# Optimization experiments

Measured on AMD Instinct MI355X. Metric: run time of the kernel, lower is better.

## Reference

```python
import jax, jax.numpy as jnp
import numpy as np

MEM_SIZE = 1_000_000
DIM = 128
BS = 256
K = 1024
TEMP = 0.07
MOM_V = 0.5
MOM_A = 0.5


def _l2norm(x, axis=-1, eps=1e-12):
    n = jnp.sqrt(jnp.sum(x * x, axis=axis, keepdims=True))
    return x / jnp.maximum(n, eps)


def setup_inputs() -> dict:
    key = jax.random.key(0)
    k1, k2, k3, k4, k5, k6 = jax.random.split(key, 6)
    video_emb = jax.random.normal(k1, (BS, DIM), dtype=jnp.float32)
    audio_emb = jax.random.normal(k2, (BS, DIM), dtype=jnp.float32)
    y = jax.random.randint(k3, (BS,), 0, MEM_SIZE, dtype=jnp.int32)
    # alias method draws over memory_size-1 items (before shifting past y)
    neg_idx = jax.random.randint(k4, (BS, K), 0, MEM_SIZE - 1, dtype=jnp.int32)
    view1_mem = _l2norm(jax.random.normal(k5, (MEM_SIZE, DIM), dtype=jnp.float32))
    view2_mem = _l2norm(jax.random.normal(k6, (MEM_SIZE, DIM), dtype=jnp.float32))
    return {
        "video_emb": video_emb,
        "audio_emb": audio_emb,
        "y": y,
        "neg_idx": neg_idx,
        "view1_mem": view1_mem,
        "view2_mem": view2_mem,
    }


def reference(video_emb, audio_emb, y, neg_idx, view1_mem, view2_mem):
    v = _l2norm(video_emb, axis=1)   # [bs, dim]
    a = _l2norm(audio_emb, axis=1)   # [bs, dim]

    # shift negative indices past the positive index y (as in sample_negatives)
    idx = neg_idx + (neg_idx >= y[:, None]).astype(neg_idx.dtype)  # [bs, K]

    # gather positives / negatives from memory banks
    v_pos = view1_mem[y]           # [bs, dim]
    a_pos = view2_mem[y]           # [bs, dim]
    v_neg = view1_mem[idx]         # [bs, K, dim]
    a_neg = view2_mem[idx]         # [bs, K, dim]

    # xModal scores (wModal=False)
    v2a_pos = jnp.einsum("bd,bd->b", a_pos, v)[:, None] / TEMP    # [bs, 1]
    v2a_neg = jnp.einsum("bkd,bd->bk", a_neg, v) / TEMP           # [bs, K]
    a2v_pos = jnp.einsum("bd,bd->b", v_pos, a)[:, None] / TEMP    # [bs, 1]
    a2v_neg = jnp.einsum("bkd,bd->bk", v_neg, a) / TEMP           # [bs, K]

    scores = jnp.stack(
        [jnp.concatenate([v2a_pos, v2a_neg], axis=1),
         jnp.concatenate([a2v_pos, a2v_neg], axis=1)],
        axis=0,
    )  # [2, bs, K+1]

    # momentum scatter update of memory banks (no_grad in original)
    new1 = _l2norm(MOM_V * v_pos + (1.0 - MOM_V) * v, axis=1)
    new2 = _l2norm(MOM_A * a_pos + (1.0 - MOM_A) * a, axis=1)
    view1_new = view1_mem.at[y].set(new1)
    view2_new = view2_mem.at[y].set(new2)

    return scores, view1_new, view2_new
```

## Files before the change

### kernel.cpp

```cpp
#include <hip/hip_runtime.h>

#define MEM_SIZE 1000000
#define DIM 128
#define BS 256
#define K 1024
#define NSC (K + 1)
#define CAP 4
#define OVFCAP 32768

constexpr float INV_TEMP = 1.0f / 0.07f;
constexpr float MOM = 0.5f;

#define NB 2048
#define BT 256
#define NWAVES (NB * BT / 64)

typedef float fx4 __attribute__((ext_vector_type(4)));

#define QTAB_OFF 0
#define CNT_OFF  262144
#define SLOT_OFF 4262144
#define OVFC_OFF 20262144
#define OVF_OFF  20262400
#define WS_NEED  20524544

__device__ __forceinline__ float wave_reduce_sum(float v) {
    #pragma unroll
    for (int off = 32; off > 0; off >>= 1)
        v += __shfl_xor(v, off, 64);
    return v;
}

__global__ void normzero_kernel(const float* __restrict__ video,
                                const float* __restrict__ audio,
                                float* __restrict__ qtab,
                                int* __restrict__ counts,
                                int* __restrict__ ovf_cnt) {
    const int u = blockIdx.x;
    const int lane = threadIdx.x;
    const int b = u & (BS - 1);
    const float* src = (u < BS) ? video : audio;
    const float2 e = reinterpret_cast<const float2*>(src + b * DIM)[lane];
    const float ss = wave_reduce_sum(e.x * e.x + e.y * e.y);
    const float inv = 1.0f / fmaxf(sqrtf(ss), 1e-12f);
    reinterpret_cast<float2*>(qtab + u * DIM)[lane] =
        make_float2(e.x * inv, e.y * inv);
    for (int i = u * 64 + lane; i < MEM_SIZE; i += 512 * 64) counts[i] = 0;
    if (u == 0 && lane == 0) *ovf_cnt = 0;
}

__global__ void build_kernel(const int* __restrict__ y,
                             const int* __restrict__ neg,
                             int* __restrict__ counts,
                             int* __restrict__ slots,
                             int* __restrict__ ovf_cnt,
                             int2* __restrict__ ovf) {
    const int E = blockIdx.x * blockDim.x + threadIdx.x;
    int b, j, row;
    if (E < BS * K) {
        b = E >> 10;
        const int jj = E & 1023;
        j = jj + 1;
        const int ni = neg[b * K + jj];
        const int yb = y[b];
        row = ni + (ni >= yb ? 1 : 0);
    } else {
        b = E - BS * K;
        if (b >= BS) return;
        j = 0;
        row = y[b];
    }
    const int key = (b << 11) | j;
    const int old = atomicAdd(&counts[row], 1);
    if (old < CAP) {
        slots[row * CAP + old] = key;
    } else {
        const int p = atomicAdd(ovf_cnt, 1);
        if (p < OVFCAP) ovf[p] = make_int2(row, key);
    }
}

__global__ __launch_bounds__(BT) void main_kernel(
    const float* __restrict__ view1, const float* __restrict__ view2,
    const float* __restrict__ qtab, const int* __restrict__ counts,
    const int* __restrict__ slots,
    float* __restrict__ scores,
    fx4* __restrict__ out1, fx4* __restrict__ out2) {
    const int tid = blockIdx.x * BT + threadIdx.x;
    const int wid = tid >> 6;
    const int lane = tid & 63;
    const int half = lane >> 5;
    const int hl = lane & 31;
    const fx4* s1 = reinterpret_cast<const fx4*>(view1);
    const fx4* s2 = reinterpret_cast<const fx4*>(view2);
    const fx4* qt4 = reinterpret_cast<const fx4*>(qtab);

    const long long n4 = (long long)MEM_SIZE * DIM / 4;
    for (long long wbase = (long long)wid * 64; wbase < n4;
         wbase += (long long)NWAVES * 64) {
        const long long i = wbase + lane;
        const fx4 a = s1[i];
        const fx4 c = s2[i];
        __builtin_nontemporal_store(a, &out1[i]);
        __builtin_nontemporal_store(c, &out2[i]);

        const int row = (int)(wbase >> 5) + half;
        int cnt = counts[row];
        if (cnt > CAP) cnt = CAP;
        for (int t = 0; t < cnt; ++t) {
            const int key = slots[row * CAP + t];
            const int b = key >> 11;
            const int j = key & 2047;
            const fx4 q0 = qt4[b * 32 + hl];
            const fx4 q1 = qt4[(256 + b) * 32 + hl];
            float d0 = q0.x * c.x + q0.y * c.y + q0.z * c.z + q0.w * c.w;
            float d1 = q1.x * a.x + q1.y * a.y + q1.z * a.z + q1.w * a.w;
            #pragma unroll
            for (int off = 16; off > 0; off >>= 1) {
                d0 += __shfl_xor(d0, off, 64);
                d1 += __shfl_xor(d1, off, 64);
            }
            if (hl == 0) {
                scores[b * NSC + j] = d0 * INV_TEMP;
                scores[(256 + b) * NSC + j] = d1 * INV_TEMP;
            }
        }
    }
}

__global__ void tail_kernel(const float* __restrict__ video,
                            const float* __restrict__ audio,
                            const int* __restrict__ y,
                            const float* __restrict__ view1,
                            const float* __restrict__ view2,
                            const float* __restrict__ qtab,
                            const int* __restrict__ ovf_cnt,
                            const int2* __restrict__ ovf,
                            float* __restrict__ scores,
                            float* __restrict__ out1,
                            float* __restrict__ out2) {
    const int blk = blockIdx.x;
    const int lane = threadIdx.x;
    if (blk < 512) {
        const int bank = blk >> 8;
        const int b = blk & (BS - 1);
        const int row = y[b];
        for (int b2 = b + 1; b2 < BS; ++b2)
            if (y[b2] == row) return;
        const float* emb = (bank == 0) ? video : audio;
        const float2 e = reinterpret_cast<const float2*>(emb + b * DIM)[lane];
        const float ss = wave_reduce_sum(e.x * e.x + e.y * e.y);
        const float inv = 1.0f / fmaxf(sqrtf(ss), 1e-12f);
        const float* mem = (bank == 0) ? view1 : view2;
        const float2 xp =
            reinterpret_cast<const float2*>(mem + (size_t)row * DIM)[lane];
        float2 nv = make_float2(MOM * xp.x + (1.0f - MOM) * e.x * inv,
                                MOM * xp.y + (1.0f - MOM) * e.y * inv);
        const float ss2 = wave_reduce_sum(nv.x * nv.x + nv.y * nv.y);
        const float inv2 = 1.0f / fmaxf(sqrtf(ss2), 1e-12f);
        float* out = (bank == 0) ? out1 : out2;
        reinterpret_cast<float2*>(out + (size_t)row * DIM)[lane] =
            make_float2(nv.x * inv2, nv.y * inv2);
    } else {
        int n = *ovf_cnt;
        if (n > OVFCAP) n = OVFCAP;
        const float2* m1 = reinterpret_cast<const float2*>(view1);
        const float2* m2 = reinterpret_cast<const float2*>(view2);
        const float2* qt2 = reinterpret_cast<const float2*>(qtab);
        for (int e = blk - 512; e < n; e += 128) {
            const int2 rk = ovf[e];
            const int row = rk.x, key = rk.y;
            const int b = key >> 11, j = key & 2047;
            const float2 xa = m1[(size_t)row * 64 + lane];
            const float2 xc = m2[(size_t)row * 64 + lane];
            const float2 q0 = qt2[(size_t)b * 64 + lane];
            const float2 q1 = qt2[(size_t)(256 + b) * 64 + lane];
            float d0 = xc.x * q0.x + xc.y * q0.y;
            float d1 = xa.x * q1.x + xa.y * q1.y;
            #pragma unroll
            for (int off = 32; off > 0; off >>= 1) {
                d0 += __shfl_xor(d0, off, 64);
                d1 += __shfl_xor(d1, off, 64);
            }
            if (lane == 0) {
                scores[b * NSC + j] = d0 * INV_TEMP;
                scores[(256 + b) * NSC + j] = d1 * INV_TEMP;
            }
        }
    }
}

__global__ __launch_bounds__(256) void fb_fused(
    const float* __restrict__ video, const float* __restrict__ audio,
    const int* __restrict__ y, const int* __restrict__ neg,
    const float* __restrict__ view1, const float* __restrict__ view2,
    float* __restrict__ scores,
    fx4* __restrict__ out1, fx4* __restrict__ out2) {
    const int bid = blockIdx.x;
    const int tid = threadIdx.x;
    if ((bid & 3) == 0) {
        const int bm = bid >> 2;
        const int m = bm >> 8;
        const int b = bm & (BS - 1);
        const int lane = tid & 63;
        const int wv = tid >> 6;
        const int yb = y[b];
        const float* emb = (m == 0) ? video : audio;
        const float2 e = reinterpret_cast<const float2*>(emb + b * DIM)[lane];
        const float ss = wave_reduce_sum(e.x * e.x + e.y * e.y);
        const float inv = 1.0f / fmaxf(sqrtf(ss), 1e-12f);
        const float vx = e.x * inv, vy = e.y * inv;
        const float2* mem2 =
            reinterpret_cast<const float2*>((m == 0) ? view2 : view1);
        float* srow = scores + (size_t)bm * NSC;
        const int* nb = neg + b * K;
        const int chunk = (NSC + 3) / 4;
        const int j0 = wv * chunk;
        const int j1 = min(NSC, j0 + chunk);
        for (int j = j0; j < j1; ++j) {
            int r0;
            if (j == 0) r0 = yb;
            else { const int ni = nb[j - 1]; r0 = ni + (ni >= yb ? 1 : 0); }
            const float2 x0 = mem2[(size_t)r0 * 64 + lane];
            const float s0 = wave_reduce_sum(x0.x * vx + x0.y * vy);
            if (lane == 0) srow[j] = s0 * INV_TEMP;
        }
    } else {
        const long long n4 = (long long)MEM_SIZE * DIM / 4;
        const int cb = bid - (bid >> 2) - 1;
        const fx4* s1 = reinterpret_cast<const fx4*>(view1);
        const fx4* s2 = reinterpret_cast<const fx4*>(view2);
        long long i = (long long)cb * blockDim.x + tid;
        const long long stride = (long long)1536 * blockDim.x;
        for (; i < n4; i += stride) {
            const fx4 a = __builtin_nontemporal_load(&s1[i]);
            const fx4 c = __builtin_nontemporal_load(&s2[i]);
            __builtin_nontemporal_store(a, &out1[i]);
            __builtin_nontemporal_store(c, &out2[i]);
        }
    }
}

__global__ void fb_scatter(const float* __restrict__ video,
                           const float* __restrict__ audio,
                           const int* __restrict__ y,
                           const float* __restrict__ view1,
                           const float* __restrict__ view2,
                           float* __restrict__ out1,
                           float* __restrict__ out2) {
    const int blk = blockIdx.x;
    const int lane = threadIdx.x;
    const int bank = blk >> 8;
    const int b = blk & (BS - 1);
    const int row = y[b];
    for (int b2 = b + 1; b2 < BS; ++b2)
        if (y[b2] == row) return;
    const float* emb = (bank == 0) ? video : audio;
    const float2 e = reinterpret_cast<const float2*>(emb + b * DIM)[lane];
    const float ss = wave_reduce_sum(e.x * e.x + e.y * e.y);
    const float inv = 1.0f / fmaxf(sqrtf(ss), 1e-12f);
    const float* mem = (bank == 0) ? view1 : view2;
    const float2 xp =
        reinterpret_cast<const float2*>(mem + (size_t)row * DIM)[lane];
    float2 nv = make_float2(MOM * xp.x + (1.0f - MOM) * e.x * inv,
                            MOM * xp.y + (1.0f - MOM) * e.y * inv);
    const float ss2 = wave_reduce_sum(nv.x * nv.x + nv.y * nv.y);
    const float inv2 = 1.0f / fmaxf(sqrtf(ss2), 1e-12f);
    float* out = (bank == 0) ? out1 : out2;
    reinterpret_cast<float2*>(out + (size_t)row * DIM)[lane] =
        make_float2(nv.x * inv2, nv.y * inv2);
}

extern "C" void kernel_launch(void* const* d_in, const int* in_sizes, int n_in,
                              void* d_out, int out_size, void* d_ws, size_t ws_size,
                              hipStream_t stream) {
    const float* video = (const float*)d_in[0];
    const float* audio = (const float*)d_in[1];
    const int* y       = (const int*)d_in[2];
    const int* neg     = (const int*)d_in[3];
    const float* v1    = (const float*)d_in[4];
    const float* v2    = (const float*)d_in[5];

    float* out    = (float*)d_out;
    float* scores = out;
    float* out1   = out + 2 * BS * NSC;
    float* out2   = out1 + (size_t)MEM_SIZE * DIM;

    if (ws_size < (size_t)WS_NEED) {
        fb_fused<<<2048, 256, 0, stream>>>(video, audio, y, neg, v1, v2,
                                           scores, (fx4*)out1, (fx4*)out2);
        fb_scatter<<<512, 64, 0, stream>>>(video, audio, y, v1, v2, out1, out2);
        return;
    }

    char* ws = (char*)d_ws;
    float* qtab  = (float*)(ws + QTAB_OFF);
    int* counts  = (int*)(ws + CNT_OFF);
    int* slots   = (int*)(ws + SLOT_OFF);
    int* ovf_cnt = (int*)(ws + OVFC_OFF);
    int2* ovf    = (int2*)(ws + OVF_OFF);

    normzero_kernel<<<512, 64, 0, stream>>>(video, audio, qtab, counts, ovf_cnt);
    build_kernel<<<1025, 256, 0, stream>>>(y, neg, counts, slots, ovf_cnt, ovf);
    main_kernel<<<NB, BT, 0, stream>>>(v1, v2, qtab, counts, slots,
                                       scores, (fx4*)out1, (fx4*)out2);
    tail_kernel<<<640, 64, 0, stream>>>(video, audio, y, v1, v2, qtab,
                                        ovf_cnt, ovf, scores, out1, out2);
}
```

Baseline: 470.6 us.

## Shrink slot table to two int2 entries per row and drop counts read

Result: no change. 473.2 us (+0.6%).

```diff
diff --git a/kernel.cpp b/kernel.cpp
--- a/kernel.cpp
+++ b/kernel.cpp
@@ -5,7 +5,6 @@
 #define BS 256
 #define K 1024
 #define NSC (K + 1)
-#define CAP 4
 #define OVFCAP 32768
 
 constexpr float INV_TEMP = 1.0f / 0.07f;
@@ -19,10 +18,10 @@
 
 #define QTAB_OFF 0
 #define CNT_OFF  262144
-#define SLOT_OFF 4262144
-#define OVFC_OFF 20262144
-#define OVF_OFF  20262400
-#define WS_NEED  20524544
+#define SLOT_OFF 4456448
+#define OVFC_OFF 12845056
+#define OVF_OFF  12845312
+#define WS_NEED  13107456
 
 __device__ __forceinline__ float wave_reduce_sum(float v) {
     #pragma unroll
@@ -31,28 +30,33 @@
     return v;
 }
 
-__global__ void normzero_kernel(const float* __restrict__ video,
-                                const float* __restrict__ audio,
-                                float* __restrict__ qtab,
-                                int* __restrict__ counts,
-                                int* __restrict__ ovf_cnt) {
-    const int u = blockIdx.x;
-    const int lane = threadIdx.x;
-    const int b = u & (BS - 1);
-    const float* src = (u < BS) ? video : audio;
-    const float2 e = reinterpret_cast<const float2*>(src + b * DIM)[lane];
-    const float ss = wave_reduce_sum(e.x * e.x + e.y * e.y);
-    const float inv = 1.0f / fmaxf(sqrtf(ss), 1e-12f);
-    reinterpret_cast<float2*>(qtab + u * DIM)[lane] =
-        make_float2(e.x * inv, e.y * inv);
-    for (int i = u * 64 + lane; i < MEM_SIZE; i += 512 * 64) counts[i] = 0;
-    if (u == 0 && lane == 0) *ovf_cnt = 0;
+__global__ __launch_bounds__(BT) void setup_kernel(
+    const float* __restrict__ video, const float* __restrict__ audio,
+    float* __restrict__ qtab, int* __restrict__ counts,
+    int* __restrict__ slots_i, int* __restrict__ ovf_cnt) {
+    const int bid = blockIdx.x;
+    const int t = threadIdx.x;
+    const int tid = bid * BT + t;
+    if (bid < 128) {
+        const int u = bid * 4 + (t >> 6);
+        const int lane = t & 63;
+        const int b = u & (BS - 1);
+        const float* src = (u < BS) ? video : audio;
+        const float2 e = reinterpret_cast<const float2*>(src + b * DIM)[lane];
+        const float ss = wave_reduce_sum(e.x * e.x + e.y * e.y);
+        const float inv = 1.0f / fmaxf(sqrtf(ss), 1e-12f);
+        reinterpret_cast<float2*>(qtab + u * DIM)[lane] =
+            make_float2(e.x * inv, e.y * inv);
+    }
+    for (int i = tid; i < MEM_SIZE; i += NB * BT) counts[i] = 0;
+    for (int i = tid; i < 2 * MEM_SIZE; i += NB * BT) slots_i[i] = -1;
+    if (tid == 0) *ovf_cnt = 0;
 }
 
 __global__ void build_kernel(const int* __restrict__ y,
                              const int* __restrict__ neg,
                              int* __restrict__ counts,
-                             int* __restrict__ slots,
+                             int* __restrict__ slots_i,
                              int* __restrict__ ovf_cnt,
                              int2* __restrict__ ovf) {
     const int E = blockIdx.x * blockDim.x + threadIdx.x;
@@ -72,8 +76,8 @@
     }
     const int key = (b << 11) | j;
     const int old = atomicAdd(&counts[row], 1);
-    if (old < CAP) {
-        slots[row * CAP + old] = key;
+    if (old < 2) {
+        slots_i[row * 2 + old] = key;
     } else {
         const int p = atomicAdd(ovf_cnt, 1);
         if (p < OVFCAP) ovf[p] = make_int2(row, key);
@@ -82,8 +86,7 @@
 
 __global__ __launch_bounds__(BT) void main_kernel(
     const float* __restrict__ view1, const float* __restrict__ view2,
-    const float* __restrict__ qtab, const int* __restrict__ counts,
-    const int* __restrict__ slots,
+    const float* __restrict__ qtab, const int2* __restrict__ slots,
     float* __restrict__ scores,
     fx4* __restrict__ out1, fx4* __restrict__ out2) {
     const int tid = blockIdx.x * BT + threadIdx.x;
@@ -99,30 +102,33 @@
     for (long long wbase = (long long)wid * 64; wbase < n4;
          wbase += (long long)NWAVES * 64) {
         const long long i = wbase + lane;
-        const fx4 a = s1[i];
-        const fx4 c = s2[i];
+        const fx4 a = __builtin_nontemporal_load(&s1[i]);
+        const fx4 c = __builtin_nontemporal_load(&s2[i]);
+        const int row = (int)(wbase >> 5) + half;
+        const int2 sl = slots[row];
         __builtin_nontemporal_store(a, &out1[i]);
         __builtin_nontemporal_store(c, &out2[i]);
 
-        const int row = (int)(wbase >> 5) + half;
-        int cnt = counts[row];
-        if (cnt > CAP) cnt = CAP;
-        for (int t = 0; t < cnt; ++t) {
-            const int key = slots[row * CAP + t];
-            const int b = key >> 11;
-            const int j = key & 2047;
-            const fx4 q0 = qt4[b * 32 + hl];
-            const fx4 q1 = qt4[(256 + b) * 32 + hl];
-            float d0 = q0.x * c.x + q0.y * c.y + q0.z * c.z + q0.w * c.w;
-            float d1 = q1.x * a.x + q1.y * a.y + q1.z * a.z + q1.w * a.w;
-            #pragma unroll
-            for (int off = 16; off > 0; off >>= 1) {
-                d0 += __shfl_xor(d0, off, 64);
-                d1 += __shfl_xor(d1, off, 64);
-            }
-            if (hl == 0) {
-                scores[b * NSC + j] = d0 * INV_TEMP;
-                scores[(256 + b) * NSC + j] = d1 * INV_TEMP;
+        #pragma unroll
+        for (int t = 0; t < 2; ++t) {
+            const int key = (t == 0) ? sl.x : sl.y;
+            if (!__any(key >= 0)) break;
+            if (key >= 0) {
+                const int b = key >> 11;
+                const int j = key & 2047;
+                const fx4 q0 = qt4[b * 32 + hl];
+                const fx4 q1 = qt4[(256 + b) * 32 + hl];
+                float d0 = q0.x * c.x + q0.y * c.y + q0.z * c.z + q0.w * c.w;
+                float d1 = q1.x * a.x + q1.y * a.y + q1.z * a.z + q1.w * a.w;
+                #pragma unroll
+                for (int off = 16; off > 0; off >>= 1) {
+                    d0 += __shfl_xor(d0, off, 64);
+                    d1 += __shfl_xor(d1, off, 64);
+                }
+                if (hl == 0) {
+                    scores[b * NSC + j] = d0 * INV_TEMP;
+                    scores[(256 + b) * NSC + j] = d1 * INV_TEMP;
+                }
             }
         }
     }
@@ -296,13 +302,16 @@
     char* ws = (char*)d_ws;
     float* qtab  = (float*)(ws + QTAB_OFF);
     int* counts  = (int*)(ws + CNT_OFF);
-    int* slots   = (int*)(ws + SLOT_OFF);
+    int* slots_i = (int*)(ws + SLOT_OFF);
+    int2* slots  = (int2*)(ws + SLOT_OFF);
     int* ovf_cnt = (int*)(ws + OVFC_OFF);
     int2* ovf    = (int2*)(ws + OVF_OFF);
 
-    normzero_kernel<<<512, 64, 0, stream>>>(video, audio, qtab, counts, ovf_cnt);
-    build_kernel<<<1025, 256, 0, stream>>>(y, neg, counts, slots, ovf_cnt, ovf);
-    main_kernel<<<NB, BT, 0, stream>>>(v1, v2, qtab, counts, slots,
+    setup_kernel<<<NB, BT, 0, stream>>>(video, audio, qtab, counts,
+                                        slots_i, ovf_cnt);
+    build_kernel<<<1025, 256, 0, stream>>>(y, neg, counts, slots_i,
+                                           ovf_cnt, ovf);
+    main_kernel<<<NB, BT, 0, stream>>>(v1, v2, qtab, slots,
                                        scores, (fx4*)out1, (fx4*)out2);
     tail_kernel<<<640, 64, 0, stream>>>(video, audio, y, v1, v2, qtab,
                                         ovf_cnt, ovf, scores, out1, out2);
```
